# Optimization experiments

Measured on AMD Instinct MI355X. Metric: run time of the kernel, lower is better.

Reference implementation:

```python
import jax, jax.numpy as jnp
import numpy as np
import math


def _neighbor_stack(x):
    # x: [b, nc, w, d] -> [b, nc, 3, w, d] with zero-padded prev/next chunks
    prev = jnp.pad(x[:, :-1], ((0, 0), (1, 0), (0, 0), (0, 0)))
    nxt = jnp.pad(x[:, 1:], ((0, 0), (0, 1), (0, 0), (0, 0)))
    return jnp.stack([prev, x, nxt], axis=2)


def local_attention(q, kv, Wq, Wkv, Wo, w):
    b, L, d_model = q.shape
    d_head = Wkv.shape[1] // 2
    h = d_model // d_head
    nc = L // w

    qp = (q @ Wq).reshape(b, L, h, d_head) / math.sqrt(d_head)
    kvp = kv @ Wkv  # [b, L, 2*d_head], single shared KV head (MQA)
    k, v = kvp[..., :d_head], kvp[..., d_head:]

    cq = qp.reshape(b, nc, w, h, d_head)
    k3 = _neighbor_stack(k.reshape(b, nc, w, d_head))  # [b, nc, 3, w, d]
    v3 = _neighbor_stack(v.reshape(b, nc, w, d_head))  # [b, nc, 3, w, d]

    # scores over (prev, self, next) chunks; padded edge chunks contribute
    # zero scores (exp(0)=1 in softmax), exactly as the torch F.pad(value=0) does.
    scores = jnp.einsum('bcxhd,bcpyd->bcxhpy', cq, k3)  # [b,nc,w,h,3,w]
    probs = jax.nn.softmax(scores.reshape(b, nc, w, h, 3 * w), axis=-1)
    probs = probs.reshape(b, nc, w, h, 3, w)

    ctx = jnp.einsum('bcxhpy,bcpyd->bcxhd', probs, v3)  # [b,nc,w,h,d]
    ctx = ctx.reshape(b, L, d_model)
    return ctx @ Wo


def setup_inputs() -> dict:
    key = jax.random.key(0)
    k1, k2, k3, k4, k5 = jax.random.split(key, 5)
    b, L, d_model, n_head = 1, 4096, 1024, 16
    d_head = d_model // n_head
    scale = 0.02
    return {
        'q': jax.random.normal(k1, (b, L, d_model), dtype=jnp.float32),
        'kv': jax.random.normal(k2, (b, L, d_model), dtype=jnp.float32),
        'Wq': jax.random.normal(k3, (d_model, d_model), dtype=jnp.float32) * scale,
        'Wkv': jax.random.normal(k4, (d_model, 2 * d_head), dtype=jnp.float32) * scale,
        'Wo': jax.random.normal(k5, (d_model, d_model), dtype=jnp.float32) * scale,
        'w': 512,
    }


def reference(q, kv, Wq, Wkv, Wo, w):
    return local_attention(q, kv, Wq, Wkv, Wo, w)
```

## Files before the change

kernel.cpp:

```cpp
#include <hip/hip_runtime.h>
#include <hip/hip_bf16.h>

typedef unsigned short u16;
typedef unsigned int u32;
typedef __attribute__((ext_vector_type(8))) short bf16x8;
typedef __attribute__((ext_vector_type(4))) float f32x4;
typedef __attribute__((ext_vector_type(16))) float f32x16;
typedef __attribute__((ext_vector_type(4))) u32 u32x4;

__device__ __forceinline__ u16 f2bf(float x) {
  __hip_bfloat16 h = __float2bfloat16(x);
  return __builtin_bit_cast(u16, h);
}

__device__ __forceinline__ u32 cvtpk(float lo, float hi) {
  u32 d;
  asm("v_cvt_pk_bf16_f32 %0, %1, %2" : "=v"(d) : "v"(lo), "v"(hi));
  return d;
}

#if __has_builtin(__builtin_amdgcn_exp2f)
#define EXP2(x) __builtin_amdgcn_exp2f(x)
#else
#define EXP2(x) __expf((x) * 0.6931471805599453f)
#endif

__device__ __forceinline__ bf16x8 mk_frag(u32 a, u32 b, u32 c, u32 d) {
  u32x4 v = {a, b, c, d};
  return __builtin_bit_cast(bf16x8, v);
}

__device__ __forceinline__ f32x16 mfma32(bf16x8 a, bf16x8 b, f32x16 c) {
  return __builtin_amdgcn_mfma_f32_32x32x16_bf16(a, b, c, 0, 0, 0);
}

__device__ __forceinline__ void gload16(const void* g, void* lds) {
  __builtin_amdgcn_global_load_lds((const __attribute__((address_space(1))) void*)g,
                                   (__attribute__((address_space(3))) void*)lds, 16, 0, 0);
}

__global__ __launch_bounds__(256) void cvt_tw(const float* __restrict__ q, const float* __restrict__ kv,
                                              const float* __restrict__ Wq, const float* __restrict__ Wkv,
                                              const float* __restrict__ Wo, u16* __restrict__ qkbf,
                                              u16* __restrict__ wqt, u16* __restrict__ wkvt,
                                              u16* __restrict__ wot) {
  __shared__ float T[64][65];
  const int t = threadIdx.x;
  const int bid = blockIdx.x;
  if (bid < 4096) {
    int idx = bid * 256 + t;
    const float* src = (idx < 524288) ? q : kv;
    int li = idx & 524287;
    const float4* p = (const float4*)src + (size_t)li * 2;
    float4 a = p[0], b = p[1];
    bf16x8 vv;
    vv[0] = (short)f2bf(a.x); vv[1] = (short)f2bf(a.y);
    vv[2] = (short)f2bf(a.z); vv[3] = (short)f2bf(a.w);
    vv[4] = (short)f2bf(b.x); vv[5] = (short)f2bf(b.y);
    vv[6] = (short)f2bf(b.z); vv[7] = (short)f2bf(b.w);
    *(bf16x8*)(qkbf + (size_t)idx * 8) = vv;
    return;
  }
  const int wb = bid - 4096;
  const float* W; u16* Wt; int N, bx, by;
  if (wb < 256)      { W = Wq;  Wt = wqt;  N = 1024; bx = wb & 15; by = wb >> 4; }
  else if (wb < 512) { int b = wb - 256; W = Wo;  Wt = wot;  N = 1024; bx = b & 15; by = b >> 4; }
  else               { int b = wb - 512; W = Wkv; Wt = wkvt; N = 128;  bx = b & 1;  by = b >> 1; }
  const int K = 1024;
  const int n0 = bx * 64, k0 = by * 64;
  #pragma unroll
  for (int pass = 0; pass < 4; ++pass) {
    int r = pass * 16 + (t >> 4);
    int c = (t & 15) * 4;
    float4 v = *(const float4*)(W + (size_t)(k0 + r) * N + n0 + c);
    T[r][c] = v.x; T[r][c + 1] = v.y; T[r][c + 2] = v.z; T[r][c + 3] = v.w;
  }
  __syncthreads();
  #pragma unroll
  for (int s = 0; s < 2; ++s) {
    int n = s * 32 + (t >> 3);
    int kk = (t & 7) * 8;
    bf16x8 vv;
    #pragma unroll
    for (int i = 0; i < 8; ++i) vv[i] = (short)f2bf(T[kk + i][n]);
    *(bf16x8*)(Wt + (size_t)(n0 + n) * K + k0 + kk) = vv;
  }
}

template<int BF16OUT>
__global__ __launch_bounds__(256, 3) void gemm_bt(const u16* __restrict__ A, const u16* __restrict__ Bt,
                                                  void* __restrict__ Cout, int N, int K, float scale) {
  __shared__ __attribute__((aligned(16))) u16 As[128 * 128];
  __shared__ __attribute__((aligned(16))) u16 Bs[64 * 128];
  const int t = threadIdx.x;
  const int lane = t & 63, wv = t >> 6;
  const int g = lane >> 4, i16 = lane & 15;
  const int m0 = blockIdx.y * 128, n0 = blockIdx.x * 64;
  const int wr = wv >> 1, wc = wv & 1;
  f32x4 acc[4][2] = {};
  for (int kt = 0; kt < K; kt += 128) {
    #pragma unroll
    for (int j = 0; j < 8; ++j) {
      int p = j * 4096 + t * 16;
      int row = p >> 8;
      int lg = (p & 255) ^ ((row & 15) << 4);
      gload16(A + (size_t)(m0 + row) * K + kt + (lg >> 1), (char*)As + p);
    }
    #pragma unroll
    for (int j = 0; j < 4; ++j) {
      int p = j * 4096 + t * 16;
      int row = p >> 8;
      int lg = (p & 255) ^ ((row & 15) << 4);
      gload16(Bt + (size_t)(n0 + row) * K + kt + (lg >> 1), (char*)Bs + p);
    }
    __syncthreads();
    bf16x8 af[4][4], bfr[4][2];
    #pragma unroll
    for (int kf = 0; kf < 4; ++kf) {
      #pragma unroll
      for (int x = 0; x < 4; ++x) {
        int ra = wr * 64 + x * 16 + i16;
        af[kf][x] = *(const bf16x8*)((const char*)As + ((ra * 256 + kf * 64 + g * 16) ^ ((ra & 15) << 4)));
      }
      #pragma unroll
      for (int x = 0; x < 2; ++x) {
        int rb = wc * 32 + x * 16 + i16;
        bfr[kf][x] = *(const bf16x8*)((const char*)Bs + ((rb * 256 + kf * 64 + g * 16) ^ ((rb & 15) << 4)));
      }
    }
    #pragma unroll
    for (int kf = 0; kf < 4; ++kf)
      #pragma unroll
      for (int mi = 0; mi < 4; ++mi)
        #pragma unroll
        for (int ni = 0; ni < 2; ++ni)
          acc[mi][ni] = __builtin_amdgcn_mfma_f32_16x16x32_bf16(af[kf][mi], bfr[kf][ni], acc[mi][ni], 0, 0, 0);
    __syncthreads();
  }
  #pragma unroll
  for (int mi = 0; mi < 4; ++mi)
    #pragma unroll
    for (int ni = 0; ni < 2; ++ni)
      #pragma unroll
      for (int r = 0; r < 4; ++r) {
        size_t off = (size_t)(m0 + wr * 64 + mi * 16 + g * 4 + r) * N + (n0 + wc * 32 + ni * 16 + i16);
        float v = acc[mi][ni][r] * scale;
        if (BF16OUT) ((u16*)Cout)[off] = f2bf(v);
        else ((float*)Cout)[off] = v;
      }
}

__global__ __launch_bounds__(256, 3) void gemm_qkv(const u16* __restrict__ qbf, const u16* __restrict__ kvbf,
                                                   const u16* __restrict__ wqt, const u16* __restrict__ wkvt,
                                                   u16* __restrict__ qp, u16* __restrict__ kvp,
                                                   u16* __restrict__ vtg) {
  __shared__ __attribute__((aligned(16))) u16 As[128 * 128];
  __shared__ __attribute__((aligned(16))) u16 Bs[64 * 128];
  const int t = threadIdx.x;
  const int lane = t & 63, wv = t >> 6;
  const int g = lane >> 4, i16 = lane & 15;
  const int wr = wv >> 1, wc = wv & 1;
  const int K = 1024;
  const int bid = blockIdx.x;
  const bool iskv = bid >= 512;
  const u16* A; const u16* Bt; int m0, n0;
  if (!iskv) { A = qbf;  Bt = wqt;  m0 = (bid >> 4) * 128; n0 = (bid & 15) * 64; }
  else       { int b = bid - 512; A = kvbf; Bt = wkvt; m0 = (b >> 1) * 128; n0 = (b & 1) * 64; }
  f32x4 acc[4][2] = {};
  for (int kt = 0; kt < K; kt += 128) {
    #pragma unroll
    for (int j = 0; j < 8; ++j) {
      int p = j * 4096 + t * 16;
      int row = p >> 8;
      int lg = (p & 255) ^ ((row & 15) << 4);
      gload16(A + (size_t)(m0 + row) * K + kt + (lg >> 1), (char*)As + p);
    }
    #pragma unroll
    for (int j = 0; j < 4; ++j) {
      int p = j * 4096 + t * 16;
      int row = p >> 8;
      int lg = (p & 255) ^ ((row & 15) << 4);
      gload16(Bt + (size_t)(n0 + row) * K + kt + (lg >> 1), (char*)Bs + p);
    }
    __syncthreads();
    bf16x8 af[4][4], bfr[4][2];
    #pragma unroll
    for (int kf = 0; kf < 4; ++kf) {
      #pragma unroll
      for (int x = 0; x < 4; ++x) {
        int ra = wr * 64 + x * 16 + i16;
        af[kf][x] = *(const bf16x8*)((const char*)As + ((ra * 256 + kf * 64 + g * 16) ^ ((ra & 15) << 4)));
      }
      #pragma unroll
      for (int x = 0; x < 2; ++x) {
        int rb = wc * 32 + x * 16 + i16;
        bfr[kf][x] = *(const bf16x8*)((const char*)Bs + ((rb * 256 + kf * 64 + g * 16) ^ ((rb & 15) << 4)));
      }
    }
    #pragma unroll
    for (int kf = 0; kf < 4; ++kf)
      #pragma unroll
      for (int mi = 0; mi < 4; ++mi)
        #pragma unroll
        for (int ni = 0; ni < 2; ++ni)
          acc[mi][ni] = __builtin_amdgcn_mfma_f32_16x16x32_bf16(af[kf][mi], bfr[kf][ni], acc[mi][ni], 0, 0, 0);
    __syncthreads();
  }
  if (!iskv) {
    #pragma unroll
    for (int mi = 0; mi < 4; ++mi)
      #pragma unroll
      for (int ni = 0; ni < 2; ++ni)
        #pragma unroll
        for (int r = 0; r < 4; ++r)
          qp[(size_t)(m0 + wr * 64 + mi * 16 + g * 4 + r) * 1024 + n0 + wc * 32 + ni * 16 + i16] =
              f2bf(acc[mi][ni][r] * 0.18033688011112042f);
  } else if (n0 == 0) {
    #pragma unroll
    for (int mi = 0; mi < 4; ++mi)
      #pragma unroll
      for (int ni = 0; ni < 2; ++ni)
        #pragma unroll
        for (int r = 0; r < 4; ++r)
          kvp[(size_t)(m0 + wr * 64 + mi * 16 + g * 4 + r) * 64 + wc * 32 + ni * 16 + i16] =
              f2bf(acc[mi][ni][r]);
  } else {
    u16* CT = (u16*)As;
    #pragma unroll
    for (int mi = 0; mi < 4; ++mi)
      #pragma unroll
      for (int ni = 0; ni < 2; ++ni)
        #pragma unroll
        for (int r = 0; r < 4; ++r)
          CT[(wc * 32 + ni * 16 + i16) * 128 + wr * 64 + mi * 16 + g * 4 + r] = f2bf(acc[mi][ni][r]);
    __syncthreads();
    int d = t >> 2, c4 = t & 3;
    const u16* src = CT + d * 128 + c4 * 32;
    u16* dst = vtg + (size_t)d * 4096 + m0 + c4 * 32;
    #pragma unroll
    for (int j = 0; j < 4; ++j)
      *(bf16x8*)(dst + j * 8) = *(const bf16x8*)(src + j * 8);
  }
}

__global__ __launch_bounds__(512, 4) void attn_kernel(const u16* __restrict__ qp, const u16* __restrict__ kvp,
                                                      const u16* __restrict__ vtg, u16* __restrict__ ctx) {
  __shared__ __attribute__((aligned(16))) u16 Ks[2][2][64 * 64];
  __shared__ __attribute__((aligned(16))) u16 Vs[2][2][64 * 64];
  const int t = threadIdx.x;
  const int lane = t & 63, wv = t >> 6;
  const int g2 = wv >> 2, wq = wv & 3;
  const int tg = t & 255;
  const int hh = lane >> 5, q32 = lane & 31;
  const int bid = blockIdx.x;
  const int qt = bid & 3, hd = (bid >> 2) & 15, c = bid >> 6;
  const int q0 = c * 512 + qt * 128 + wq * 32;
  const int pk32 = (q32 & 19) | ((q32 & 4) << 1) | ((q32 & 8) >> 1);

  bf16x8 qf[4];
  #pragma unroll
  for (int dt = 0; dt < 4; ++dt)
    qf[dt] = *(const bf16x8*)(qp + (size_t)(q0 + q32) * 1024 + hd * 64 + dt * 16 + hh * 8);

  const int kb0 = (c - 1) * 512;
  const int v0 = (c == 0) ? 8 : 0;
  const int nv = (c == 0 || c == 7) ? 16 : 24;
  const int n2 = nv >> 1;
  const int s0 = v0 + g2 * n2;
  float l = g2 ? 0.f : 32.f * (float)(24 - nv);
  f32x16 accO[2] = {};

  int kA[2], vA[2];
  #pragma unroll
  for (int j = 0; j < 2; ++j) {
    int p = j * 4096 + tg * 16;
    int row = p >> 7;
    int lg = (p & 127) ^ ((row & 7) << 4);
    kA[j] = row * 64 + (lg >> 1);
    vA[j] = row * 4096 + (lg >> 1);
  }

  auto stage = [&](int b, int tile) {
    const int kb = kb0 + tile * 64;
    #pragma unroll
    for (int j = 0; j < 2; ++j)
      gload16(kvp + (size_t)(kb * 64 + kA[j]), (char*)Ks[g2][b] + j * 4096 + tg * 16);
    #pragma unroll
    for (int j = 0; j < 2; ++j)
      gload16(vtg + (size_t)(kb + vA[j]), (char*)Vs[g2][b] + j * 4096 + tg * 16);
  };

  stage(0, s0);

  for (int i = 0; i < n2; ++i) {
    asm volatile("s_waitcnt vmcnt(0)" ::: "memory");
    __builtin_amdgcn_s_barrier();
    if (i + 1 < n2) stage((i + 1) & 1, s0 + i + 1);
    const char* kbase0 = (const char*)Ks[g2][i & 1];
    const char* vbase0 = (const char*)Vs[g2][i & 1];
    f32x16 s[2] = {};
    #pragma unroll
    for (int kt = 0; kt < 2; ++kt) {
      const char* kbase = kbase0 + kt * 4096 + pk32 * 128;
      int kswz = (pk32 & 7) << 4;
      #pragma unroll
      for (int dt = 0; dt < 4; ++dt) {
        bf16x8 kf = *(const bf16x8*)(kbase + ((dt * 32 + hh * 16) ^ kswz));
        s[kt] = mfma32(kf, qf[dt], s[kt]);
      }
    }
    #pragma unroll
    for (int kt = 0; kt < 2; ++kt) {
      #pragma unroll
      for (int r = 0; r < 16; ++r) s[kt][r] = EXP2(s[kt][r]);
      l += (((s[kt][0] + s[kt][1]) + (s[kt][2] + s[kt][3])) + ((s[kt][4] + s[kt][5]) + (s[kt][6] + s[kt][7]))) +
           (((s[kt][8] + s[kt][9]) + (s[kt][10] + s[kt][11])) + ((s[kt][12] + s[kt][13]) + (s[kt][14] + s[kt][15])));
      u32 w[8];
      #pragma unroll
      for (int j = 0; j < 8; ++j) w[j] = cvtpk(s[kt][2 * j], s[kt][2 * j + 1]);
      bf16x8 pb0 = mk_frag(w[0], w[1], w[2], w[3]);
      bf16x8 pb1 = mk_frag(w[4], w[5], w[6], w[7]);
      int vswz = (q32 & 7) << 4;
      #pragma unroll
      for (int dtv = 0; dtv < 2; ++dtv) {
        const char* vbase = vbase0 + dtv * 4096 + q32 * 128;
        bf16x8 va0 = *(const bf16x8*)(vbase + ((kt * 64 + hh * 16) ^ vswz));
        accO[dtv] = mfma32(va0, pb0, accO[dtv]);
        bf16x8 va1 = *(const bf16x8*)(vbase + ((kt * 64 + 32 + hh * 16) ^ vswz));
        accO[dtv] = mfma32(va1, pb1, accO[dtv]);
      }
    }
  }

  __syncthreads();
  char* M = (char*)&Ks[0][0][0];
  float* Lx = (float*)&Vs[0][0][0];
  if (g2 == 1) {
    #pragma unroll
    for (int dtv = 0; dtv < 2; ++dtv)
      #pragma unroll
      for (int j = 0; j < 4; ++j) {
        f32x4 chunk = {accO[dtv][4 * j], accO[dtv][4 * j + 1], accO[dtv][4 * j + 2], accO[dtv][4 * j + 3]};
        int byte = lane * 128 + dtv * 64 + j * 16;
        *(f32x4*)(M + wq * 8192 + (byte ^ ((lane & 7) << 4))) = chunk;
      }
    Lx[wq * 64 + lane] = l;
  }
  __syncthreads();
  if (g2 == 0) {
    #pragma unroll
    for (int dtv = 0; dtv < 2; ++dtv)
      #pragma unroll
      for (int j = 0; j < 4; ++j) {
        int byte = lane * 128 + dtv * 64 + j * 16;
        f32x4 chunk = *(const f32x4*)(M + wq * 8192 + (byte ^ ((lane & 7) << 4)));
        #pragma unroll
        for (int e = 0; e < 4; ++e) accO[dtv][4 * j + e] += chunk[e];
      }
    l += Lx[wq * 64 + lane];
    l += __shfl_xor(l, 32);
    float rl = 1.0f / l;
    char* Ow = (char*)&Vs[1][0][0] + wq * 4096;
    #pragma unroll
    for (int dtv = 0; dtv < 2; ++dtv)
      #pragma unroll
      for (int j = 0; j < 4; ++j) {
        int d = dtv * 32 + 8 * j + 4 * hh;
        uint2 wp;
        wp.x = cvtpk(accO[dtv][4 * j] * rl, accO[dtv][4 * j + 1] * rl);
        wp.y = cvtpk(accO[dtv][4 * j + 2] * rl, accO[dtv][4 * j + 3] * rl);
        *(uint2*)(Ow + q32 * 128 + ((d * 2) ^ ((q32 & 7) << 4))) = wp;
      }
    asm volatile("s_waitcnt lgkmcnt(0)" ::: "memory");
    __builtin_amdgcn_sched_barrier(0);
    #pragma unroll
    for (int rep = 0; rep < 4; ++rep) {
      int q = lane >> 1, dblk = (lane & 1) * 4 + rep, d0 = dblk * 8;
      bf16x8 ov = *(const bf16x8*)(Ow + q * 128 + ((d0 * 2) ^ ((q & 7) << 4)));
      *(bf16x8*)(ctx + (size_t)(q0 + q) * 1024 + hd * 64 + d0) = ov;
    }
  }
}

extern "C" void kernel_launch(void* const* d_in, const int* in_sizes, int n_in,
                              void* d_out, int out_size, void* d_ws, size_t ws_size,
                              hipStream_t stream) {
  const float* q   = (const float*)d_in[0];
  const float* kv  = (const float*)d_in[1];
  const float* Wq  = (const float*)d_in[2];
  const float* Wkv = (const float*)d_in[3];
  const float* Wo  = (const float*)d_in[4];
  char* ws = (char*)d_ws;
  u16* qbf  = (u16*)(ws);
  u16* ctx  = (u16*)(ws);
  u16* kvbf = (u16*)(ws + 8388608);
  u16* qp   = (u16*)(ws + 16777216);
  u16* kvp  = (u16*)(ws + 25165824);
  u16* vtg  = (u16*)(ws + 25690112);
  u16* wqt  = (u16*)(ws + 26214400);
  u16* wkvt = (u16*)(ws + 28311552);
  u16* wot  = (u16*)(ws + 28573696);
  cvt_tw<<<4640, 256, 0, stream>>>(q, kv, Wq, Wkv, Wo, qbf, wqt, wkvt, wot);
  gemm_qkv<<<576, 256, 0, stream>>>(qbf, kvbf, wqt, wkvt, qp, kvp, vtg);
  attn_kernel<<<512, 512, 0, stream>>>(qp, kvp, vtg, ctx);
  gemm_bt<0><<<dim3(16, 32), 256, 0, stream>>>(ctx, wot, (float*)d_out, 1024, 1024, 1.0f);
}
```

Measured before the change: 85.88 us.

## Have each attention wave process two 32-query tiles to reuse K/V fragments

The attention block drops from 8 waves to 4, and each wave now computes two 32-row query tiles (A and B) against the same K and V LDS fragments. This halves LDS reads of K/V per query and doubles MFMA work per load. Staging is redistributed across the 128 threads of each group, and the cross-group reduction and output writeback are rewritten for two accumulator sets. The cost is more registers per wave, fewer waves per block, and a launch bound of 2 blocks per CU, which may reduce latency hiding.

```diff
diff --git a/kernel.cpp b/kernel.cpp
--- a/kernel.cpp
+++ b/kernel.cpp
@@ -243,37 +243,40 @@
   }
 }
 
-__global__ __launch_bounds__(512, 4) void attn_kernel(const u16* __restrict__ qp, const u16* __restrict__ kvp,
+__global__ __launch_bounds__(256, 2) void attn_kernel(const u16* __restrict__ qp, const u16* __restrict__ kvp,
                                                       const u16* __restrict__ vtg, u16* __restrict__ ctx) {
   __shared__ __attribute__((aligned(16))) u16 Ks[2][2][64 * 64];
   __shared__ __attribute__((aligned(16))) u16 Vs[2][2][64 * 64];
   const int t = threadIdx.x;
   const int lane = t & 63, wv = t >> 6;
-  const int g2 = wv >> 2, wq = wv & 3;
-  const int tg = t & 255;
+  const int g2 = wv >> 1, wq = wv & 1;
+  const int tg = t & 127;
   const int hh = lane >> 5, q32 = lane & 31;
   const int bid = blockIdx.x;
   const int qt = bid & 3, hd = (bid >> 2) & 15, c = bid >> 6;
-  const int q0 = c * 512 + qt * 128 + wq * 32;
+  const int q0 = c * 512 + qt * 128 + wq * 64;
   const int pk32 = (q32 & 19) | ((q32 & 4) << 1) | ((q32 & 8) >> 1);
 
-  bf16x8 qf[4];
+  bf16x8 qfA[4], qfB[4];
   #pragma unroll
-  for (int dt = 0; dt < 4; ++dt)
-    qf[dt] = *(const bf16x8*)(qp + (size_t)(q0 + q32) * 1024 + hd * 64 + dt * 16 + hh * 8);
+  for (int dt = 0; dt < 4; ++dt) {
+    qfA[dt] = *(const bf16x8*)(qp + (size_t)(q0 + q32) * 1024 + hd * 64 + dt * 16 + hh * 8);
+    qfB[dt] = *(const bf16x8*)(qp + (size_t)(q0 + 32 + q32) * 1024 + hd * 64 + dt * 16 + hh * 8);
+  }
 
   const int kb0 = (c - 1) * 512;
   const int v0 = (c == 0) ? 8 : 0;
   const int nv = (c == 0 || c == 7) ? 16 : 24;
   const int n2 = nv >> 1;
   const int s0 = v0 + g2 * n2;
-  float l = g2 ? 0.f : 32.f * (float)(24 - nv);
-  f32x16 accO[2] = {};
-
-  int kA[2], vA[2];
+  const float lpad = g2 ? 0.f : 32.f * (float)(24 - nv);
+  float lA = lpad, lB = lpad;
+  f32x16 accA[2] = {}, accB[2] = {};
+
+  int kA[4], vA[4];
   #pragma unroll
-  for (int j = 0; j < 2; ++j) {
-    int p = j * 4096 + tg * 16;
+  for (int j = 0; j < 4; ++j) {
+    int p = j * 2048 + tg * 16;
     int row = p >> 7;
     int lg = (p & 127) ^ ((row & 7) << 4);
     kA[j] = row * 64 + (lg >> 1);
@@ -283,11 +286,11 @@
   auto stage = [&](int b, int tile) {
     const int kb = kb0 + tile * 64;
     #pragma unroll
-    for (int j = 0; j < 2; ++j)
-      gload16(kvp + (size_t)(kb * 64 + kA[j]), (char*)Ks[g2][b] + j * 4096 + tg * 16);
-    #pragma unroll
-    for (int j = 0; j < 2; ++j)
-      gload16(vtg + (size_t)(kb + vA[j]), (char*)Vs[g2][b] + j * 4096 + tg * 16);
+    for (int j = 0; j < 4; ++j)
+      gload16(kvp + (size_t)(kb * 64 + kA[j]), (char*)Ks[g2][b] + j * 2048 + tg * 16);
+    #pragma unroll
+    for (int j = 0; j < 4; ++j)
+      gload16(vtg + (size_t)(kb + vA[j]), (char*)Vs[g2][b] + j * 2048 + tg * 16);
   };
 
   stage(0, s0);
@@ -298,7 +301,7 @@
     if (i + 1 < n2) stage((i + 1) & 1, s0 + i + 1);
     const char* kbase0 = (const char*)Ks[g2][i & 1];
     const char* vbase0 = (const char*)Vs[g2][i & 1];
-    f32x16 s[2] = {};
+    f32x16 sA[2] = {}, sB[2] = {};
     #pragma unroll
     for (int kt = 0; kt < 2; ++kt) {
       const char* kbase = kbase0 + kt * 4096 + pk32 * 128;
@@ -306,78 +309,99 @@
       #pragma unroll
       for (int dt = 0; dt < 4; ++dt) {
         bf16x8 kf = *(const bf16x8*)(kbase + ((dt * 32 + hh * 16) ^ kswz));
-        s[kt] = mfma32(kf, qf[dt], s[kt]);
+        sA[kt] = mfma32(kf, qfA[dt], sA[kt]);
+        sB[kt] = mfma32(kf, qfB[dt], sB[kt]);
       }
     }
     #pragma unroll
     for (int kt = 0; kt < 2; ++kt) {
       #pragma unroll
-      for (int r = 0; r < 16; ++r) s[kt][r] = EXP2(s[kt][r]);
-      l += (((s[kt][0] + s[kt][1]) + (s[kt][2] + s[kt][3])) + ((s[kt][4] + s[kt][5]) + (s[kt][6] + s[kt][7]))) +
-           (((s[kt][8] + s[kt][9]) + (s[kt][10] + s[kt][11])) + ((s[kt][12] + s[kt][13]) + (s[kt][14] + s[kt][15])));
-      u32 w[8];
-      #pragma unroll
-      for (int j = 0; j < 8; ++j) w[j] = cvtpk(s[kt][2 * j], s[kt][2 * j + 1]);
-      bf16x8 pb0 = mk_frag(w[0], w[1], w[2], w[3]);
-      bf16x8 pb1 = mk_frag(w[4], w[5], w[6], w[7]);
+      for (int r = 0; r < 16; ++r) sA[kt][r] = EXP2(sA[kt][r]);
+      #pragma unroll
+      for (int r = 0; r < 16; ++r) sB[kt][r] = EXP2(sB[kt][r]);
+      lA += (((sA[kt][0] + sA[kt][1]) + (sA[kt][2] + sA[kt][3])) + ((sA[kt][4] + sA[kt][5]) + (sA[kt][6] + sA[kt][7]))) +
+            (((sA[kt][8] + sA[kt][9]) + (sA[kt][10] + sA[kt][11])) + ((sA[kt][12] + sA[kt][13]) + (sA[kt][14] + sA[kt][15])));
+      lB += (((sB[kt][0] + sB[kt][1]) + (sB[kt][2] + sB[kt][3])) + ((sB[kt][4] + sB[kt][5]) + (sB[kt][6] + sB[kt][7]))) +
+            (((sB[kt][8] + sB[kt][9]) + (sB[kt][10] + sB[kt][11])) + ((sB[kt][12] + sB[kt][13]) + (sB[kt][14] + sB[kt][15])));
+      u32 wA[8], wB[8];
+      #pragma unroll
+      for (int j = 0; j < 8; ++j) wA[j] = cvtpk(sA[kt][2 * j], sA[kt][2 * j + 1]);
+      #pragma unroll
+      for (int j = 0; j < 8; ++j) wB[j] = cvtpk(sB[kt][2 * j], sB[kt][2 * j + 1]);
+      bf16x8 pbA0 = mk_frag(wA[0], wA[1], wA[2], wA[3]);
+      bf16x8 pbA1 = mk_frag(wA[4], wA[5], wA[6], wA[7]);
+      bf16x8 pbB0 = mk_frag(wB[0], wB[1], wB[2], wB[3]);
+      bf16x8 pbB1 = mk_frag(wB[4], wB[5], wB[6], wB[7]);
       int vswz = (q32 & 7) << 4;
       #pragma unroll
       for (int dtv = 0; dtv < 2; ++dtv) {
         const char* vbase = vbase0 + dtv * 4096 + q32 * 128;
         bf16x8 va0 = *(const bf16x8*)(vbase + ((kt * 64 + hh * 16) ^ vswz));
-        accO[dtv] = mfma32(va0, pb0, accO[dtv]);
+        accA[dtv] = mfma32(va0, pbA0, accA[dtv]);
+        accB[dtv] = mfma32(va0, pbB0, accB[dtv]);
         bf16x8 va1 = *(const bf16x8*)(vbase + ((kt * 64 + 32 + hh * 16) ^ vswz));
-        accO[dtv] = mfma32(va1, pb1, accO[dtv]);
+        accA[dtv] = mfma32(va1, pbA1, accA[dtv]);
+        accB[dtv] = mfma32(va1, pbB1, accB[dtv]);
       }
     }
   }
 
   __syncthreads();
   char* M = (char*)&Ks[0][0][0];
-  float* Lx = (float*)&Vs[0][0][0];
+  float* Lx = (float*)((char*)&Vs[0][0][0] + 24576);
   if (g2 == 1) {
     #pragma unroll
-    for (int dtv = 0; dtv < 2; ++dtv)
-      #pragma unroll
-      for (int j = 0; j < 4; ++j) {
-        f32x4 chunk = {accO[dtv][4 * j], accO[dtv][4 * j + 1], accO[dtv][4 * j + 2], accO[dtv][4 * j + 3]};
-        int byte = lane * 128 + dtv * 64 + j * 16;
-        *(f32x4*)(M + wq * 8192 + (byte ^ ((lane & 7) << 4))) = chunk;
-      }
-    Lx[wq * 64 + lane] = l;
+    for (int set = 0; set < 2; ++set) {
+      const f32x16* ac = set ? accB : accA;
+      #pragma unroll
+      for (int dtv = 0; dtv < 2; ++dtv)
+        #pragma unroll
+        for (int j = 0; j < 4; ++j) {
+          f32x4 chunk = {ac[dtv][4 * j], ac[dtv][4 * j + 1], ac[dtv][4 * j + 2], ac[dtv][4 * j + 3]};
+          int byte = lane * 128 + dtv * 64 + j * 16;
+          *(f32x4*)(M + wq * 16384 + set * 8192 + (byte ^ ((lane & 7) << 4))) = chunk;
+        }
+      Lx[(wq * 2 + set) * 64 + lane] = set ? lB : lA;
+    }
   }
   __syncthreads();
   if (g2 == 0) {
     #pragma unroll
-    for (int dtv = 0; dtv < 2; ++dtv)
-      #pragma unroll
-      for (int j = 0; j < 4; ++j) {
-        int byte = lane * 128 + dtv * 64 + j * 16;
-        f32x4 chunk = *(const f32x4*)(M + wq * 8192 + (byte ^ ((lane & 7) << 4)));
-        #pragma unroll
-        for (int e = 0; e < 4; ++e) accO[dtv][4 * j + e] += chunk[e];
-      }
-    l += Lx[wq * 64 + lane];
-    l += __shfl_xor(l, 32);
-    float rl = 1.0f / l;
-    char* Ow = (char*)&Vs[1][0][0] + wq * 4096;
-    #pragma unroll
-    for (int dtv = 0; dtv < 2; ++dtv)
-      #pragma unroll
-      for (int j = 0; j < 4; ++j) {
-        int d = dtv * 32 + 8 * j + 4 * hh;
-        uint2 wp;
-        wp.x = cvtpk(accO[dtv][4 * j] * rl, accO[dtv][4 * j + 1] * rl);
-        wp.y = cvtpk(accO[dtv][4 * j + 2] * rl, accO[dtv][4 * j + 3] * rl);
-        *(uint2*)(Ow + q32 * 128 + ((d * 2) ^ ((q32 & 7) << 4))) = wp;
-      }
-    asm volatile("s_waitcnt lgkmcnt(0)" ::: "memory");
-    __builtin_amdgcn_sched_barrier(0);
-    #pragma unroll
-    for (int rep = 0; rep < 4; ++rep) {
-      int q = lane >> 1, dblk = (lane & 1) * 4 + rep, d0 = dblk * 8;
-      bf16x8 ov = *(const bf16x8*)(Ow + q * 128 + ((d0 * 2) ^ ((q & 7) << 4)));
-      *(bf16x8*)(ctx + (size_t)(q0 + q) * 1024 + hd * 64 + d0) = ov;
+    for (int set = 0; set < 2; ++set) {
+      f32x16* ac = set ? accB : accA;
+      #pragma unroll
+      for (int dtv = 0; dtv < 2; ++dtv)
+        #pragma unroll
+        for (int j = 0; j < 4; ++j) {
+          int byte = lane * 128 + dtv * 64 + j * 16;
+          f32x4 chunk = *(const f32x4*)(M + wq * 16384 + set * 8192 + (byte ^ ((lane & 7) << 4)));
+          #pragma unroll
+          for (int e = 0; e < 4; ++e) ac[dtv][4 * j + e] += chunk[e];
+        }
+      float l = (set ? lB : lA) + Lx[(wq * 2 + set) * 64 + lane];
+      l += __shfl_xor(l, 32);
+      float rl = 1.0f / l;
+      char* Ow = (char*)&Vs[0][0][0] + wq * 4096;
+      #pragma unroll
+      for (int dtv = 0; dtv < 2; ++dtv)
+        #pragma unroll
+        for (int j = 0; j < 4; ++j) {
+          int d = dtv * 32 + 8 * j + 4 * hh;
+          uint2 wp;
+          wp.x = cvtpk(ac[dtv][4 * j] * rl, ac[dtv][4 * j + 1] * rl);
+          wp.y = cvtpk(ac[dtv][4 * j + 2] * rl, ac[dtv][4 * j + 3] * rl);
+          *(uint2*)(Ow + q32 * 128 + ((d * 2) ^ ((q32 & 7) << 4))) = wp;
+        }
+      asm volatile("s_waitcnt lgkmcnt(0)" ::: "memory");
+      __builtin_amdgcn_sched_barrier(0);
+      #pragma unroll
+      for (int rep = 0; rep < 4; ++rep) {
+        int q = lane >> 1, dblk = (lane & 1) * 4 + rep, d0 = dblk * 8;
+        bf16x8 ov = *(const bf16x8*)(Ow + q * 128 + ((d0 * 2) ^ ((q & 7) << 4)));
+        *(bf16x8*)(ctx + (size_t)(q0 + set * 32 + q) * 1024 + hd * 64 + d0) = ov;
+      }
+      asm volatile("s_waitcnt lgkmcnt(0) vmcnt(0)" ::: "memory");
+      __builtin_amdgcn_sched_barrier(0);
     }
   }
 }
@@ -402,6 +426,6 @@
   u16* wot  = (u16*)(ws + 28573696);
   cvt_tw<<<4640, 256, 0, stream>>>(q, kv, Wq, Wkv, Wo, qbf, wqt, wkvt, wot);
   gemm_qkv<<<576, 256, 0, stream>>>(qbf, kvbf, wqt, wkvt, qp, kvp, vtg);
-  attn_kernel<<<512, 512, 0, stream>>>(qp, kvp, vtg, ctx);
+  attn_kernel<<<512, 256, 0, stream>>>(qp, kvp, vtg, ctx);
   gemm_bt<0><<<dim3(16, 32), 256, 0, stream>>>(ctx, wot, (float*)d_out, 1024, 1024, 1.0f);
 }
```

After: 84.07 us. 1.02x faster.
